# Performance work log

Hardware: AMD Instinct MI355X
Metric: run time of the kernel (lower is better)

The kernel has to match this reference:

```python
import jax, jax.numpy as jnp
import numpy as np

B, C, H, W = 8, 256, 64, 64
RED = 8
GAMMA = 1.0

def setup_inputs() -> dict:
    key = jax.random.key(0)
    k0, k1, k2, k3 = jax.random.split(key, 4)
    Cr = C // RED
    scale = 1.0 / np.sqrt(C).astype(np.float32)
    x = jax.random.normal(k0, (B, C, H, W), jnp.float32)
    # 1x1 conv weights (no bias) == channel-mixing matrices [out_c, in_c]
    w1 = jax.random.normal(k1, (Cr, C), jnp.float32) * scale  # query proj
    w2 = jax.random.normal(k2, (Cr, C), jnp.float32) * scale  # key proj
    w3 = jax.random.normal(k3, (C, C), jnp.float32) * scale   # value proj
    return {"x": x, "w1": w1, "w2": w2, "w3": w3}

def reference(x, w1, w2, w3):
    b, c, h, w = x.shape
    n = h * w
    xf = x.reshape(b, c, n)                      # [B,C,N]  (hw_flattern)
    f = jnp.einsum('oc,bcn->bon', w1, xf)        # [B,Cr,N] conv1 (1x1)
    g = jnp.einsum('oc,bcn->bon', w2, xf)        # [B,Cr,N] conv2 (1x1)
    hh = jnp.einsum('oc,bcn->bon', w3, xf)       # [B,C,N]  conv3 (1x1)
    # s = f^T g : [B,N,N]
    s = jnp.einsum('bki,bkj->bij', f, g)
    # NOTE: torch softmax over dim=1 (rows), not the usual last dim
    beta = jax.nn.softmax(s, axis=1)             # [B,N,N]
    o = jnp.einsum('bck,bkn->bcn', hh, beta)     # [B,C,N]
    o = o.reshape(b, c, h, w)
    return GAMMA * o + x
```

## Files before the change

### kernel.cpp

```cpp
#include <hip/hip_runtime.h>
#include <stdint.h>

#define Bsz 8
#define Cc  256
#define Crr 32
#define Nn  4096
#define CN  (Cc * Nn)
#define ITILE 128
#define NIT (Nn / ITILE)
#define PPITCH 136
#define YPITCH 264

typedef unsigned short u16;
typedef __attribute__((ext_vector_type(8))) short  short8;
typedef __attribute__((ext_vector_type(4))) float  floatx4;
typedef __attribute__((ext_vector_type(4))) unsigned short u16x4;

__device__ __forceinline__ floatx4 mfma16(short8 a, short8 b, floatx4 c) {
  return __builtin_amdgcn_mfma_f32_16x16x32_bf16(a, b, c, 0, 0, 0);
}
__device__ __forceinline__ u16 f2bf(float f) {
  unsigned int u = __builtin_bit_cast(unsigned int, f);
  u = (u + 0x7FFFu + ((u >> 16) & 1u)) >> 16;
  return (u16)u;
}
__device__ __forceinline__ float bf2f(u16 h) {
  unsigned int u = ((unsigned int)h) << 16;
  return __builtin_bit_cast(float, u);
}
__device__ __forceinline__ short8 pack8(const float* __restrict__ p) {
  floatx4 a = *(const floatx4*)p;
  floatx4 b = *(const floatx4*)(p + 4);
  short8 r;
  r[0] = (short)f2bf(a[0]); r[1] = (short)f2bf(a[1]);
  r[2] = (short)f2bf(a[2]); r[3] = (short)f2bf(a[3]);
  r[4] = (short)f2bf(b[0]); r[5] = (short)f2bf(b[1]);
  r[6] = (short)f2bf(b[2]); r[7] = (short)f2bf(b[3]);
  return r;
}
__device__ __forceinline__ void split8(const float* __restrict__ p,
                                       short8& hi, short8& lo) {
  floatx4 a = *(const floatx4*)p;
  floatx4 b = *(const floatx4*)(p + 4);
  float v[8] = {a[0], a[1], a[2], a[3], b[0], b[1], b[2], b[3]};
#pragma unroll
  for (int r = 0; r < 8; ++r) {
    u16 h = f2bf(v[r]);
    hi[r] = (short)h;
    lo[r] = (short)f2bf(v[r] - bf2f(h));
  }
}

template <bool XB16>
__launch_bounds__(256, 4)
__global__ void proj_kernel(const float* __restrict__ x,
                            const float* __restrict__ w1,
                            const float* __restrict__ w2,
                            const float* __restrict__ w3,
                            u16* __restrict__ w3b,
                            u16* __restrict__ fThi, u16* __restrict__ fTlo,
                            u16* __restrict__ gThi, u16* __restrict__ gTlo,
                            u16* __restrict__ xb) {
  const int bid = blockIdx.x;
  const int b   = bid & 7;
  const int nt  = bid >> 3;
  const int tid  = threadIdx.x;
  const int w    = tid >> 6;
  const int lane = tid & 63;
  const int m    = lane & 15;
  const int q    = lane >> 4;
  const int nhalf = w >> 1;
  const int chalf = w & 1;
  const int nb   = nt * 32 + nhalf * 16;

  __shared__ float comb[2][16][64];

  const float* xsl = x + (size_t)b * CN;
  const floatx4 z4 = {0.f, 0.f, 0.f, 0.f};
  floatx4 aF[2] = {z4, z4}, aG[2] = {z4, z4};

  for (int ci = 0; ci < 4; ++ci) {
    const int c0 = chalf * 128 + ci * 32;
    const float* xp = xsl + (size_t)(c0 + q * 8) * Nn + nb + m;
    short8 xh, xl;
#pragma unroll
    for (int r = 0; r < 8; ++r) {
      float v = xp[(size_t)r * Nn];
      u16 h = f2bf(v);
      xh[r] = (short)h;
      xl[r] = (short)f2bf(v - bf2f(h));
    }
    if (XB16) {
      const int n  = nb + m;
      const int it = n >> 5;
      const int nq = ((n & 31) >> 3) << 4;
      const int el = n & 7;
      const size_t tb = (size_t)b * CN;
#pragma unroll
      for (int r = 0; r < 8; ++r) {
        int c = c0 + q * 8 + r;
        xb[tb + ((size_t)((it * 16 + (c >> 4)) << 9)) + ((c & 15) + nq) * 8 + el] =
            (u16)xh[r];
      }
    }
#pragma unroll
    for (int ot = 0; ot < 2; ++ot) {
      short8 wh, wl;
      split8(w1 + (size_t)(ot * 16 + m) * Cc + c0 + q * 8, wh, wl);
      aF[ot] = mfma16(xh, wh, aF[ot]);
      aF[ot] = mfma16(xh, wl, aF[ot]);
      aF[ot] = mfma16(xl, wh, aF[ot]);
      split8(w2 + (size_t)(ot * 16 + m) * Cc + c0 + q * 8, wh, wl);
      aG[ot] = mfma16(xh, wh, aG[ot]);
      aG[ot] = mfma16(xh, wl, aG[ot]);
      aG[ot] = mfma16(xl, wh, aG[ot]);
    }
  }

  if (chalf) {
#pragma unroll
    for (int k = 0; k < 2; ++k)
#pragma unroll
      for (int r = 0; r < 4; ++r) {
        comb[nhalf][k * 4 + r][lane]     = aF[k][r];
        comb[nhalf][8 + k * 4 + r][lane] = aG[k][r];
      }
  }
  __syncthreads();
  if (!chalf) {
#pragma unroll
    for (int ot = 0; ot < 2; ++ot)
#pragma unroll
      for (int r = 0; r < 4; ++r) {
        float vf = aF[ot][r] + comb[nhalf][ot * 4 + r][lane];
        float vg = aG[ot][r] + comb[nhalf][8 + ot * 4 + r][lane];
        int n = nb + q * 4 + r;
        size_t idx = ((size_t)b * Nn + n) * Crr + ot * 16 + m;
        u16 hf = f2bf(vf);
        fThi[idx] = hf;
        fTlo[idx] = f2bf(vf - bf2f(hf));
        u16 hg = f2bf(vg);
        gThi[idx] = hg;
        gTlo[idx] = f2bf(vg - bf2f(hg));
      }
  }
  if (bid < 64) {
    int base = bid * 1024 + tid * 4;
    floatx4 v = *(const floatx4*)(w3 + base);
    u16x4 o;
    o[0] = f2bf(v[0]); o[1] = f2bf(v[1]); o[2] = f2bf(v[2]); o[3] = f2bf(v[3]);
    *(u16x4*)(w3b + base) = o;
  }
}

template <bool XB16>
__launch_bounds__(512, 4)
__global__ void attn_kernel(const u16* __restrict__ fThi,
                            const u16* __restrict__ fTlo,
                            const u16* __restrict__ gThi,
                            const u16* __restrict__ gTlo,
                            const u16* __restrict__ xb,
                            const float* __restrict__ x,
                            const u16* __restrict__ w3b,
                            float* __restrict__ out) {
  const int bid = blockIdx.x;
  const int b   = bid & 7;
  const int jt  = bid >> 3;
  const int j0  = jt * 64;
  const int tid  = threadIdx.x;
  const int w    = tid >> 6;
  const int lane = tid & 63;
  const int m    = lane & 15;
  const int q    = lane >> 4;

  __shared__ u16   P[2 * 64 * PPITCH];
  __shared__ float lred[32 * 64];
  __shared__ float linv[64];

  const size_t fgb = (size_t)b * (size_t)Nn * Crr;
  const u16*   xbs = xb + (size_t)b * CN;
  const float* xfs = x + (size_t)b * CN;

  short8 bgh[4], bgl[4];
#pragma unroll
  for (int jb = 0; jb < 4; ++jb) {
    size_t idx = fgb + (size_t)(j0 + jb * 16 + m) * Crr + q * 8;
    bgh[jb] = *(const short8*)(gThi + idx);
    bgl[jb] = *(const short8*)(gTlo + idx);
  }

  const floatx4 z4 = {0.f, 0.f, 0.f, 0.f};
  floatx4 acc[2][4];
#pragma unroll
  for (int cb = 0; cb < 2; ++cb)
#pragma unroll
    for (int jb = 0; jb < 4; ++jb) acc[cb][jb] = z4;

  float ps[4] = {0.f, 0.f, 0.f, 0.f};
  unsigned int pw[4][2];

  auto computeS = [&](int t) {
    const int ig = t * ITILE + w * 16 + m;
    size_t fidx = fgb + (size_t)ig * Crr + q * 8;
    short8 afh = *(const short8*)(fThi + fidx);
    short8 afl = *(const short8*)(fTlo + fidx);
#pragma unroll
    for (int jb = 0; jb < 4; ++jb) {
      floatx4 t3 = mfma16(afl, bgh[jb], z4);
      t3 = mfma16(afh, bgl[jb], t3);
      t3 = mfma16(afh, bgh[jb], t3);
      u16 h0 = f2bf(__expf(t3[0]));
      u16 h1 = f2bf(__expf(t3[1]));
      u16 h2 = f2bf(__expf(t3[2]));
      u16 h3 = f2bf(__expf(t3[3]));
      ps[jb] += (bf2f(h0) + bf2f(h1)) + (bf2f(h2) + bf2f(h3));
      pw[jb][0] = (unsigned int)h0 | ((unsigned int)h1 << 16);
      pw[jb][1] = (unsigned int)h2 | ((unsigned int)h3 << 16);
    }
  };

  computeS(0);

  for (int t = 0; t < NIT; ++t) {
    u16* buf = P + (t & 1) * (64 * PPITCH);
    const int gr = w * 2 + (q >> 1);
#pragma unroll
    for (int jb = 0; jb < 4; ++jb) {
      const int j = jb * 16 + m;
      *(uint2*)(buf + j * PPITCH + gr * 8 + (q & 1) * 4) =
          make_uint2(pw[jb][0], pw[jb][1]);
    }
    __syncthreads();

    if (t + 1 < NIT) computeS(t + 1);

#pragma unroll
    for (int kk = 0; kk < 4; ++kk) {
      short8 bp[4];
#pragma unroll
      for (int jb = 0; jb < 4; ++jb)
        bp[jb] = *(const short8*)(buf + (jb * 16 + m) * PPITCH + (kk * 4 + q) * 8);
#pragma unroll
      for (int cb = 0; cb < 2; ++cb) {
        short8 ah;
        if (XB16) {
          const int tile = (t * 4 + kk) * 16 + (w * 2 + cb);
          ah = *(const short8*)(xbs + ((size_t)tile << 9) + lane * 8);
        } else {
          ah = pack8(xfs + (size_t)((w * 2 + cb) * 16 + m) * Nn +
                     t * ITILE + kk * 32 + q * 8);
        }
#pragma unroll
        for (int jb = 0; jb < 4; ++jb)
          acc[cb][jb] = mfma16(ah, bp[jb], acc[cb][jb]);
      }
    }
  }

#pragma unroll
  for (int jb = 0; jb < 4; ++jb)
    lred[(w * 4 + q) * 64 + jb * 16 + m] = ps[jb];
  __syncthreads();
  if (tid < 64) {
    float s = 0.f;
#pragma unroll
    for (int t2 = 0; t2 < 32; ++t2) s += lred[t2 * 64 + tid];
    linv[tid] = 1.0f / s;
  }
  __syncthreads();

  u16* yt = P;
#pragma unroll
  for (int cb = 0; cb < 2; ++cb)
#pragma unroll
    for (int jb = 0; jb < 4; ++jb) {
      const int j = jb * 16 + m;
      const float li = linv[j];
      unsigned int d0 = (unsigned int)f2bf(acc[cb][jb][0] * li) |
                        ((unsigned int)f2bf(acc[cb][jb][1] * li) << 16);
      unsigned int d1 = (unsigned int)f2bf(acc[cb][jb][2] * li) |
                        ((unsigned int)f2bf(acc[cb][jb][3] * li) << 16);
      *(uint2*)(yt + j * YPITCH + (w * 2 + cb) * 16 + q * 4) = make_uint2(d0, d1);
    }
  __syncthreads();

  floatx4 macc[2][4];
#pragma unroll
  for (int ct = 0; ct < 2; ++ct)
#pragma unroll
    for (int jb = 0; jb < 4; ++jb) macc[ct][jb] = z4;

  for (int k0 = 0; k0 < Cc; k0 += 32) {
    short8 bf_[4];
#pragma unroll
    for (int jb = 0; jb < 4; ++jb)
      bf_[jb] = *(const short8*)(yt + (jb * 16 + m) * YPITCH + k0 + q * 8);
#pragma unroll
    for (int ct = 0; ct < 2; ++ct) {
      short8 aw = *(const short8*)(w3b + (size_t)((w * 2 + ct) * 16 + m) * Cc +
                                   k0 + q * 8);
#pragma unroll
      for (int jb = 0; jb < 4; ++jb)
        macc[ct][jb] = mfma16(aw, bf_[jb], macc[ct][jb]);
    }
  }

  float* osl = out + (size_t)b * CN;
#pragma unroll
  for (int ct = 0; ct < 2; ++ct)
#pragma unroll
    for (int jb = 0; jb < 4; ++jb)
#pragma unroll
      for (int r = 0; r < 4; ++r) {
        const int c = (w * 2 + ct) * 16 + q * 4 + r;
        const size_t idx = (size_t)c * Nn + j0 + jb * 16 + m;
        osl[idx] = macc[ct][jb][r] + xfs[idx];
      }
}

extern "C" void kernel_launch(void* const* d_in, const int* in_sizes, int n_in,
                              void* d_out, int out_size, void* d_ws, size_t ws_size,
                              hipStream_t stream) {
  const float* x  = (const float*)d_in[0];
  const float* w1 = (const float*)d_in[1];
  const float* w2 = (const float*)d_in[2];
  const float* w3 = (const float*)d_in[3];
  float* out = (float*)d_out;

  const size_t FG = (size_t)Bsz * Nn * Crr;
  u16* w3b  = (u16*)d_ws;
  u16* fThi = w3b + (size_t)Cc * Cc;
  u16* fTlo = fThi + FG;
  u16* gThi = fTlo + FG;
  u16* gTlo = gThi + FG;
  u16* xb   = gTlo + FG;
  const size_t need_xb = ((size_t)Cc * Cc + 4 * FG + (size_t)Bsz * CN) * 2;
  const bool use_xb = ws_size >= need_xb;

  if (use_xb) {
    proj_kernel<true><<<dim3(1024), dim3(256), 0, stream>>>(
        x, w1, w2, w3, w3b, fThi, fTlo, gThi, gTlo, xb);
    attn_kernel<true><<<dim3(512), dim3(512), 0, stream>>>(
        fThi, fTlo, gThi, gTlo, xb, x, w3b, out);
  } else {
    proj_kernel<false><<<dim3(1024), dim3(256), 0, stream>>>(
        x, w1, w2, w3, w3b, fThi, fTlo, gThi, gTlo, xb);
    attn_kernel<false><<<dim3(512), dim3(512), 0, stream>>>(
        fThi, fTlo, gThi, gTlo, xb, x, w3b, out);
  }
}
```

Measured before the change: 234.6 us.

## Halve attention column tile to 32 with 4-wave blocks and relayout xb tiles

The attention kernel now handles 32 output columns per block with 256 threads (4 waves), launching 1024 blocks instead of 512. Each wave covers 64 channels and 32 rows of i per step, so the per-wave MFMA work is reshaped. The bf16 copy of x is stored in a new per-tile layout (row-major 16x32) and read with matching offsets. More blocks should give better CU occupancy and load balance. The cost is that the exp/S work is now computed for half as many columns per block, so each x tile is read twice as often overall.

```diff
diff --git a/kernel.cpp b/kernel.cpp
--- a/kernel.cpp
+++ b/kernel.cpp
@@ -8,6 +8,7 @@
 #define CN  (Cc * Nn)
 #define ITILE 128
 #define NIT (Nn / ITILE)
+#define JT  32
 #define PPITCH 136
 #define YPITCH 264
 
@@ -91,16 +92,13 @@
       xl[r] = (short)f2bf(v - bf2f(h));
     }
     if (XB16) {
-      const int n  = nb + m;
-      const int it = n >> 5;
-      const int nq = ((n & 31) >> 3) << 4;
-      const int el = n & 7;
+      const int n = nb + m;
       const size_t tb = (size_t)b * CN;
 #pragma unroll
       for (int r = 0; r < 8; ++r) {
         int c = c0 + q * 8 + r;
-        xb[tb + ((size_t)((it * 16 + (c >> 4)) << 9)) + ((c & 15) + nq) * 8 + el] =
-            (u16)xh[r];
+        xb[tb + ((size_t)((n >> 5) * 16 + (c >> 4)) << 9) +
+           (c & 15) * 32 + (n & 31)] = (u16)xh[r];
       }
     }
 #pragma unroll
@@ -154,7 +152,7 @@
 }
 
 template <bool XB16>
-__launch_bounds__(512, 4)
+__launch_bounds__(256, 4)
 __global__ void attn_kernel(const u16* __restrict__ fThi,
                             const u16* __restrict__ fTlo,
                             const u16* __restrict__ gThi,
@@ -166,69 +164,75 @@
   const int bid = blockIdx.x;
   const int b   = bid & 7;
   const int jt  = bid >> 3;
-  const int j0  = jt * 64;
+  const int j0  = jt * JT;
   const int tid  = threadIdx.x;
   const int w    = tid >> 6;
   const int lane = tid & 63;
   const int m    = lane & 15;
   const int q    = lane >> 4;
 
-  __shared__ u16   P[2 * 64 * PPITCH];
-  __shared__ float lred[32 * 64];
-  __shared__ float linv[64];
+  __shared__ u16   P[2 * JT * PPITCH];
+  __shared__ float lred[16 * JT];
+  __shared__ float linv[JT];
 
   const size_t fgb = (size_t)b * (size_t)Nn * Crr;
   const u16*   xbs = xb + (size_t)b * CN;
   const float* xfs = x + (size_t)b * CN;
 
-  short8 bgh[4], bgl[4];
-#pragma unroll
-  for (int jb = 0; jb < 4; ++jb) {
+  short8 bgh[2], bgl[2];
+#pragma unroll
+  for (int jb = 0; jb < 2; ++jb) {
     size_t idx = fgb + (size_t)(j0 + jb * 16 + m) * Crr + q * 8;
     bgh[jb] = *(const short8*)(gThi + idx);
     bgl[jb] = *(const short8*)(gTlo + idx);
   }
 
   const floatx4 z4 = {0.f, 0.f, 0.f, 0.f};
-  floatx4 acc[2][4];
-#pragma unroll
-  for (int cb = 0; cb < 2; ++cb)
-#pragma unroll
-    for (int jb = 0; jb < 4; ++jb) acc[cb][jb] = z4;
-
-  float ps[4] = {0.f, 0.f, 0.f, 0.f};
-  unsigned int pw[4][2];
+  floatx4 acc[4][2];
+#pragma unroll
+  for (int cb = 0; cb < 4; ++cb)
+#pragma unroll
+    for (int jb = 0; jb < 2; ++jb) acc[cb][jb] = z4;
+
+  float ps[2] = {0.f, 0.f};
+  unsigned int pw[2][2][2];
 
   auto computeS = [&](int t) {
-    const int ig = t * ITILE + w * 16 + m;
-    size_t fidx = fgb + (size_t)ig * Crr + q * 8;
-    short8 afh = *(const short8*)(fThi + fidx);
-    short8 afl = *(const short8*)(fTlo + fidx);
-#pragma unroll
-    for (int jb = 0; jb < 4; ++jb) {
-      floatx4 t3 = mfma16(afl, bgh[jb], z4);
-      t3 = mfma16(afh, bgl[jb], t3);
-      t3 = mfma16(afh, bgh[jb], t3);
-      u16 h0 = f2bf(__expf(t3[0]));
-      u16 h1 = f2bf(__expf(t3[1]));
-      u16 h2 = f2bf(__expf(t3[2]));
-      u16 h3 = f2bf(__expf(t3[3]));
-      ps[jb] += (bf2f(h0) + bf2f(h1)) + (bf2f(h2) + bf2f(h3));
-      pw[jb][0] = (unsigned int)h0 | ((unsigned int)h1 << 16);
-      pw[jb][1] = (unsigned int)h2 | ((unsigned int)h3 << 16);
+#pragma unroll
+    for (int isub = 0; isub < 2; ++isub) {
+      const int ig = t * ITILE + w * 32 + isub * 16 + m;
+      size_t fidx = fgb + (size_t)ig * Crr + q * 8;
+      short8 afh = *(const short8*)(fThi + fidx);
+      short8 afl = *(const short8*)(fTlo + fidx);
+#pragma unroll
+      for (int jb = 0; jb < 2; ++jb) {
+        floatx4 t3 = mfma16(afl, bgh[jb], z4);
+        t3 = mfma16(afh, bgl[jb], t3);
+        t3 = mfma16(afh, bgh[jb], t3);
+        u16 h0 = f2bf(__expf(t3[0]));
+        u16 h1 = f2bf(__expf(t3[1]));
+        u16 h2 = f2bf(__expf(t3[2]));
+        u16 h3 = f2bf(__expf(t3[3]));
+        ps[jb] += (bf2f(h0) + bf2f(h1)) + (bf2f(h2) + bf2f(h3));
+        pw[isub][jb][0] = (unsigned int)h0 | ((unsigned int)h1 << 16);
+        pw[isub][jb][1] = (unsigned int)h2 | ((unsigned int)h3 << 16);
+      }
     }
   };
 
   computeS(0);
 
   for (int t = 0; t < NIT; ++t) {
-    u16* buf = P + (t & 1) * (64 * PPITCH);
-    const int gr = w * 2 + (q >> 1);
-#pragma unroll
-    for (int jb = 0; jb < 4; ++jb) {
-      const int j = jb * 16 + m;
-      *(uint2*)(buf + j * PPITCH + gr * 8 + (q & 1) * 4) =
-          make_uint2(pw[jb][0], pw[jb][1]);
+    u16* buf = P + (t & 1) * (JT * PPITCH);
+#pragma unroll
+    for (int isub = 0; isub < 2; ++isub) {
+      const int gr = w * 4 + isub * 2 + (q >> 1);
+#pragma unroll
+      for (int jb = 0; jb < 2; ++jb) {
+        const int j = jb * 16 + m;
+        *(uint2*)(buf + j * PPITCH + gr * 8 + (q & 1) * 4) =
+            make_uint2(pw[isub][jb][0], pw[isub][jb][1]);
+      }
     }
     __syncthreads();
 
@@ -236,83 +240,83 @@
 
 #pragma unroll
     for (int kk = 0; kk < 4; ++kk) {
-      short8 bp[4];
-#pragma unroll
-      for (int jb = 0; jb < 4; ++jb)
+      short8 bp[2];
+#pragma unroll
+      for (int jb = 0; jb < 2; ++jb)
         bp[jb] = *(const short8*)(buf + (jb * 16 + m) * PPITCH + (kk * 4 + q) * 8);
 #pragma unroll
-      for (int cb = 0; cb < 2; ++cb) {
+      for (int cb = 0; cb < 4; ++cb) {
         short8 ah;
         if (XB16) {
-          const int tile = (t * 4 + kk) * 16 + (w * 2 + cb);
-          ah = *(const short8*)(xbs + ((size_t)tile << 9) + lane * 8);
+          const int tile = (t * 4 + kk) * 16 + (w * 4 + cb);
+          ah = *(const short8*)(xbs + ((size_t)tile << 9) + m * 32 + q * 8);
         } else {
-          ah = pack8(xfs + (size_t)((w * 2 + cb) * 16 + m) * Nn +
+          ah = pack8(xfs + (size_t)((w * 4 + cb) * 16 + m) * Nn +
                      t * ITILE + kk * 32 + q * 8);
         }
 #pragma unroll
-        for (int jb = 0; jb < 4; ++jb)
+        for (int jb = 0; jb < 2; ++jb)
           acc[cb][jb] = mfma16(ah, bp[jb], acc[cb][jb]);
       }
     }
   }
 
 #pragma unroll
-  for (int jb = 0; jb < 4; ++jb)
-    lred[(w * 4 + q) * 64 + jb * 16 + m] = ps[jb];
+  for (int jb = 0; jb < 2; ++jb)
+    lred[(w * 4 + q) * JT + jb * 16 + m] = ps[jb];
   __syncthreads();
-  if (tid < 64) {
+  if (tid < JT) {
     float s = 0.f;
 #pragma unroll
-    for (int t2 = 0; t2 < 32; ++t2) s += lred[t2 * 64 + tid];
+    for (int t2 = 0; t2 < 16; ++t2) s += lred[t2 * JT + tid];
     linv[tid] = 1.0f / s;
   }
   __syncthreads();
 
   u16* yt = P;
 #pragma unroll
-  for (int cb = 0; cb < 2; ++cb)
-#pragma unroll
-    for (int jb = 0; jb < 4; ++jb) {
+  for (int cb = 0; cb < 4; ++cb)
+#pragma unroll
+    for (int jb = 0; jb < 2; ++jb) {
       const int j = jb * 16 + m;
       const float li = linv[j];
       unsigned int d0 = (unsigned int)f2bf(acc[cb][jb][0] * li) |
                         ((unsigned int)f2bf(acc[cb][jb][1] * li) << 16);
       unsigned int d1 = (unsigned int)f2bf(acc[cb][jb][2] * li) |
                         ((unsigned int)f2bf(acc[cb][jb][3] * li) << 16);
-      *(uint2*)(yt + j * YPITCH + (w * 2 + cb) * 16 + q * 4) = make_uint2(d0, d1);
+      *(uint2*)(yt + j * YPITCH + (w * 4 + cb) * 16 + q * 4) = make_uint2(d0, d1);
     }
   __syncthreads();
 
-  floatx4 macc[2][4];
-#pragma unroll
-  for (int ct = 0; ct < 2; ++ct)
-#pragma unroll
-    for (int jb = 0; jb < 4; ++jb) macc[ct][jb] = z4;
+  floatx4 macc[4][2];
+#pragma unroll
+  for (int ct = 0; ct < 4; ++ct)
+#pragma unroll
+    for (int jb = 0; jb < 2; ++jb) macc[ct][jb] = z4;
 
   for (int k0 = 0; k0 < Cc; k0 += 32) {
-    short8 bf_[4];
-#pragma unroll
-    for (int jb = 0; jb < 4; ++jb)
+    short8 bf_[2];
+#pragma unroll
+    for (int jb = 0; jb < 2; ++jb)
       bf_[jb] = *(const short8*)(yt + (jb * 16 + m) * YPITCH + k0 + q * 8);
 #pragma unroll
-    for (int ct = 0; ct < 2; ++ct) {
-      short8 aw = *(const short8*)(w3b + (size_t)((w * 2 + ct) * 16 + m) * Cc +
+    for (int ct = 0; ct < 4; ++ct) {
+      short8 aw = *(const short8*)(w3b + (size_t)((w * 4 + ct) * 16 + m) * Cc +
                                    k0 + q * 8);
 #pragma unroll
-      for (int jb = 0; jb < 4; ++jb)
+      for (int jb = 0; jb < 2; ++jb)
         macc[ct][jb] = mfma16(aw, bf_[jb], macc[ct][jb]);
     }
   }
 
   float* osl = out + (size_t)b * CN;
 #pragma unroll
-  for (int ct = 0; ct < 2; ++ct)
-#pragma unroll
-    for (int jb = 0; jb < 4; ++jb)
+  for (int ct = 0; ct < 4; ++ct)
+#pragma unroll
+    for (int jb = 0; jb < 2; ++jb)
 #pragma unroll
       for (int r = 0; r < 4; ++r) {
-        const int c = (w * 2 + ct) * 16 + q * 4 + r;
+        const int c = (w * 4 + ct) * 16 + q * 4 + r;
         const size_t idx = (size_t)c * Nn + j0 + jb * 16 + m;
         osl[idx] = macc[ct][jb][r] + xfs[idx];
       }
@@ -340,12 +344,12 @@
   if (use_xb) {
     proj_kernel<true><<<dim3(1024), dim3(256), 0, stream>>>(
         x, w1, w2, w3, w3b, fThi, fTlo, gThi, gTlo, xb);
-    attn_kernel<true><<<dim3(512), dim3(512), 0, stream>>>(
+    attn_kernel<true><<<dim3(1024), dim3(256), 0, stream>>>(
         fThi, fTlo, gThi, gTlo, xb, x, w3b, out);
   } else {
     proj_kernel<false><<<dim3(1024), dim3(256), 0, stream>>>(
         x, w1, w2, w3, w3b, fThi, fTlo, gThi, gTlo, xb);
-    attn_kernel<false><<<dim3(512), dim3(512), 0, stream>>>(
+    attn_kernel<false><<<dim3(1024), dim3(256), 0, stream>>>(
         fThi, fTlo, gThi, gTlo, xb, x, w3b, out);
   }
 }
```

Measured after the change: 272.0 us. 1.16x slower.

## Interleave next-tile score computation with PV MFMAs and split projection channels four ways

Applied to the files above, without the earlier changes.

The attention loop no longer computes the next tile's scores in one block after the barrier. It prefetches the f fragments two tiles ahead and issues each jb slice of the S/exp computation inside the kk loop, so exp and VALU work interleave with the value MFMAs. The projection kernel now splits channels across four waves over 16 columns, reduces three partials through shared memory, and launches twice as many blocks. The xb tile layout changes to row-major 16x32 and the reader is updated to match. This costs extra registers for the prefetched fragments and a peeled final iteration.

```diff
diff --git a/kernel.cpp b/kernel.cpp
--- a/kernel.cpp
+++ b/kernel.cpp
@@ -69,18 +69,16 @@
   const int lane = tid & 63;
   const int m    = lane & 15;
   const int q    = lane >> 4;
-  const int nhalf = w >> 1;
-  const int chalf = w & 1;
-  const int nb   = nt * 32 + nhalf * 16;
-
-  __shared__ float comb[2][16][64];
+  const int nb   = nt * 16;
+
+  __shared__ float comb[3][16][64];
 
   const float* xsl = x + (size_t)b * CN;
   const floatx4 z4 = {0.f, 0.f, 0.f, 0.f};
   floatx4 aF[2] = {z4, z4}, aG[2] = {z4, z4};
 
-  for (int ci = 0; ci < 4; ++ci) {
-    const int c0 = chalf * 128 + ci * 32;
+  for (int ci = 0; ci < 2; ++ci) {
+    const int c0 = w * 64 + ci * 32;
     const float* xp = xsl + (size_t)(c0 + q * 8) * Nn + nb + m;
     short8 xh, xl;
 #pragma unroll
@@ -91,16 +89,13 @@
       xl[r] = (short)f2bf(v - bf2f(h));
     }
     if (XB16) {
-      const int n  = nb + m;
-      const int it = n >> 5;
-      const int nq = ((n & 31) >> 3) << 4;
-      const int el = n & 7;
+      const int n = nb + m;
       const size_t tb = (size_t)b * CN;
 #pragma unroll
       for (int r = 0; r < 8; ++r) {
         int c = c0 + q * 8 + r;
-        xb[tb + ((size_t)((it * 16 + (c >> 4)) << 9)) + ((c & 15) + nq) * 8 + el] =
-            (u16)xh[r];
+        xb[tb + ((size_t)((n >> 5) * 16 + (c >> 4)) << 9) +
+           (c & 15) * 32 + (n & 31)] = (u16)xh[r];
       }
     }
 #pragma unroll
@@ -117,23 +112,25 @@
     }
   }
 
-  if (chalf) {
+  if (w > 0) {
 #pragma unroll
     for (int k = 0; k < 2; ++k)
 #pragma unroll
       for (int r = 0; r < 4; ++r) {
-        comb[nhalf][k * 4 + r][lane]     = aF[k][r];
-        comb[nhalf][8 + k * 4 + r][lane] = aG[k][r];
+        comb[w - 1][k * 4 + r][lane]     = aF[k][r];
+        comb[w - 1][8 + k * 4 + r][lane] = aG[k][r];
       }
   }
   __syncthreads();
-  if (!chalf) {
+  if (w == 0) {
 #pragma unroll
     for (int ot = 0; ot < 2; ++ot)
 #pragma unroll
       for (int r = 0; r < 4; ++r) {
-        float vf = aF[ot][r] + comb[nhalf][ot * 4 + r][lane];
-        float vg = aG[ot][r] + comb[nhalf][8 + ot * 4 + r][lane];
+        float vf = aF[ot][r] + comb[0][ot * 4 + r][lane] +
+                   comb[1][ot * 4 + r][lane] + comb[2][ot * 4 + r][lane];
+        float vg = aG[ot][r] + comb[0][8 + ot * 4 + r][lane] +
+                   comb[1][8 + ot * 4 + r][lane] + comb[2][8 + ot * 4 + r][lane];
         int n = nb + q * 4 + r;
         size_t idx = ((size_t)b * Nn + n) * Crr + ot * 16 + m;
         u16 hf = f2bf(vf);
@@ -198,32 +195,35 @@
 
   float ps[4] = {0.f, 0.f, 0.f, 0.f};
   unsigned int pw[4][2];
-
-  auto computeS = [&](int t) {
-    const int ig = t * ITILE + w * 16 + m;
-    size_t fidx = fgb + (size_t)ig * Crr + q * 8;
-    short8 afh = *(const short8*)(fThi + fidx);
-    short8 afl = *(const short8*)(fTlo + fidx);
-#pragma unroll
-    for (int jb = 0; jb < 4; ++jb) {
-      floatx4 t3 = mfma16(afl, bgh[jb], z4);
-      t3 = mfma16(afh, bgl[jb], t3);
-      t3 = mfma16(afh, bgh[jb], t3);
-      u16 h0 = f2bf(__expf(t3[0]));
-      u16 h1 = f2bf(__expf(t3[1]));
-      u16 h2 = f2bf(__expf(t3[2]));
-      u16 h3 = f2bf(__expf(t3[3]));
-      ps[jb] += (bf2f(h0) + bf2f(h1)) + (bf2f(h2) + bf2f(h3));
-      pw[jb][0] = (unsigned int)h0 | ((unsigned int)h1 << 16);
-      pw[jb][1] = (unsigned int)h2 | ((unsigned int)h3 << 16);
-    }
+  short8 fAh, fAl, fBh, fBl;
+
+  auto sPart = [&](int jb) {
+    floatx4 t3 = mfma16(fAl, bgh[jb], z4);
+    t3 = mfma16(fAh, bgl[jb], t3);
+    t3 = mfma16(fAh, bgh[jb], t3);
+    u16 h0 = f2bf(__expf(t3[0]));
+    u16 h1 = f2bf(__expf(t3[1]));
+    u16 h2 = f2bf(__expf(t3[2]));
+    u16 h3 = f2bf(__expf(t3[3]));
+    ps[jb] += (bf2f(h0) + bf2f(h1)) + (bf2f(h2) + bf2f(h3));
+    pw[jb][0] = (unsigned int)h0 | ((unsigned int)h1 << 16);
+    pw[jb][1] = (unsigned int)h2 | ((unsigned int)h3 << 16);
   };
 
-  computeS(0);
-
-  for (int t = 0; t < NIT; ++t) {
+  {
+    size_t fidx = fgb + (size_t)(w * 16 + m) * Crr + q * 8;
+    fAh = *(const short8*)(fThi + fidx);
+    fAl = *(const short8*)(fTlo + fidx);
+#pragma unroll
+    for (int jb = 0; jb < 4; ++jb) sPart(jb);
+    size_t f1 = fgb + (size_t)(ITILE + w * 16 + m) * Crr + q * 8;
+    fAh = *(const short8*)(fThi + f1);
+    fAl = *(const short8*)(fTlo + f1);
+  }
+
+  const int gr = w * 2 + (q >> 1);
+  for (int t = 0; t < NIT - 1; ++t) {
     u16* buf = P + (t & 1) * (64 * PPITCH);
-    const int gr = w * 2 + (q >> 1);
 #pragma unroll
     for (int jb = 0; jb < 4; ++jb) {
       const int j = jb * 16 + m;
@@ -232,7 +232,11 @@
     }
     __syncthreads();
 
-    if (t + 1 < NIT) computeS(t + 1);
+    if (t + 2 < NIT) {
+      size_t fidx = fgb + (size_t)((t + 2) * ITILE + w * 16 + m) * Crr + q * 8;
+      fBh = *(const short8*)(fThi + fidx);
+      fBl = *(const short8*)(fTlo + fidx);
+    }
 
 #pragma unroll
     for (int kk = 0; kk < 4; ++kk) {
@@ -245,9 +249,44 @@
         short8 ah;
         if (XB16) {
           const int tile = (t * 4 + kk) * 16 + (w * 2 + cb);
-          ah = *(const short8*)(xbs + ((size_t)tile << 9) + lane * 8);
+          ah = *(const short8*)(xbs + ((size_t)tile << 9) + m * 32 + q * 8);
         } else {
-          ah = pack8(xfs + (size_t)((w * 2 + cb) * 16 + m) * Nn +
+          ah = pack8(xfs + (size_t)(((w * 2 + cb) * 16 + m)) * Nn +
+                     t * ITILE + kk * 32 + q * 8);
+        }
+#pragma unroll
+        for (int jb = 0; jb < 4; ++jb)
+          acc[cb][jb] = mfma16(ah, bp[jb], acc[cb][jb]);
+      }
+      sPart(kk);
+    }
+    fAh = fBh; fAl = fBl;
+  }
+
+  {
+    const int t = NIT - 1;
+    u16* buf = P + (t & 1) * (64 * PPITCH);
+#pragma unroll
+    for (int jb = 0; jb < 4; ++jb) {
+      const int j = jb * 16 + m;
+      *(uint2*)(buf + j * PPITCH + gr * 8 + (q & 1) * 4) =
+          make_uint2(pw[jb][0], pw[jb][1]);
+    }
+    __syncthreads();
+#pragma unroll
+    for (int kk = 0; kk < 4; ++kk) {
+      short8 bp[4];
+#pragma unroll
+      for (int jb = 0; jb < 4; ++jb)
+        bp[jb] = *(const short8*)(buf + (jb * 16 + m) * PPITCH + (kk * 4 + q) * 8);
+#pragma unroll
+      for (int cb = 0; cb < 2; ++cb) {
+        short8 ah;
+        if (XB16) {
+          const int tile = (t * 4 + kk) * 16 + (w * 2 + cb);
+          ah = *(const short8*)(xbs + ((size_t)tile << 9) + m * 32 + q * 8);
+        } else {
+          ah = pack8(xfs + (size_t)(((w * 2 + cb) * 16 + m)) * Nn +
                      t * ITILE + kk * 32 + q * 8);
         }
 #pragma unroll
@@ -338,12 +377,12 @@
   const bool use_xb = ws_size >= need_xb;
 
   if (use_xb) {
-    proj_kernel<true><<<dim3(1024), dim3(256), 0, stream>>>(
+    proj_kernel<true><<<dim3(2048), dim3(256), 0, stream>>>(
         x, w1, w2, w3, w3b, fThi, fTlo, gThi, gTlo, xb);
     attn_kernel<true><<<dim3(512), dim3(512), 0, stream>>>(
         fThi, fTlo, gThi, gTlo, xb, x, w3b, out);
   } else {
-    proj_kernel<false><<<dim3(1024), dim3(256), 0, stream>>>(
+    proj_kernel<false><<<dim3(2048), dim3(256), 0, stream>>>(
         x, w1, w2, w3, w3b, fThi, fTlo, gThi, gTlo, xb);
     attn_kernel<false><<<dim3(512), dim3(512), 0, stream>>>(
         fThi, fTlo, gThi, gTlo, xb, x, w3b, out);
```

Result: faster. 216.0 us (-7.9%).
